# Kernel optimization log

Measured on AMD Instinct MI355X. Metric: run time of the kernel, lower is better.

## Reference

```python
import jax, jax.numpy as jnp
import numpy as np

FFT_NORM = "forward"


def _deq_cplx(qp, scale, mn):
    # qp stores (q_int8 + 127) in [0, 254]; dequant: qp*scale + min, last dim = (re, im)
    f = qp.astype(jnp.float32) * scale + mn
    return jax.lax.complex(f[..., 0], f[..., 1])


def setup_inputs() -> dict:
    key = jax.random.key(0)
    ks = jax.random.split(key, 16)
    B, Cin, Cout, H, W = 8, 32, 32, 256, 256
    NxW, NyW = 32, 17            # half-modes of the spectral weight
    r0, r1, r2, r3 = 16, 16, 16, 9  # Tucker ranks
    inp = {
        "x": jax.random.normal(ks[0], (B, Cin, H, W), dtype=jnp.float32),
        "core_scale": jax.random.uniform(ks[1], (), jnp.float32, 0.001, 0.02),
        "core_min": jax.random.normal(ks[2], (), jnp.float32) * 0.1,
        "factor_scales": jax.random.uniform(ks[3], (4,), jnp.float32, 0.001, 0.02),
        "factor_mins": jax.random.normal(ks[4], (4,), jnp.float32) * 0.1,
        "b_scale": jax.random.uniform(ks[5], (), jnp.float32, 0.001, 0.02),
        "b_min": jax.random.normal(ks[6], (), jnp.float32) * 0.1,
        "q_core": jax.random.randint(ks[7], (r0, r1, r2, r3, 2), 0, 255, jnp.int32),
        "q_f0": jax.random.randint(ks[8], (Cin, r0, 2), 0, 255, jnp.int32),
        "q_f1": jax.random.randint(ks[9], (Cout, r1, 2), 0, 255, jnp.int32),
        "q_f2": jax.random.randint(ks[10], (NxW, r2, 2), 0, 255, jnp.int32),
        "q_f3": jax.random.randint(ks[11], (NyW, r3, 2), 0, 255, jnp.int32),
        "q_bias": jax.random.randint(ks[12], (Cout,), 0, 255, jnp.int32),
    }
    return inp


def reference(x, core_scale, core_min, factor_scales, factor_mins, b_scale, b_min,
              q_core, q_f0, q_f1, q_f2, q_f3, q_bias):
    # 1) rFFT over the last two (spatial) dims
    x_fft = jnp.fft.rfftn(x, axes=(-2, -1), norm=FFT_NORM)  # [B, Cin, Nx, Ny_r] c64

    # 2) dequantize Tucker core + factors, reconstruct complex weight via multi_mode_dot
    core = _deq_cplx(q_core, core_scale, core_min)                       # [r0,r1,r2,r3]
    F0 = _deq_cplx(q_f0, factor_scales[0], factor_mins[0])               # [Cin, r0]
    F1 = _deq_cplx(q_f1, factor_scales[1], factor_mins[1])               # [Cout, r1]
    F2 = _deq_cplx(q_f2, factor_scales[2], factor_mins[2])               # [NxW, r2]
    F3 = _deq_cplx(q_f3, factor_scales[3], factor_mins[3])               # [NyW, r3]
    W = jnp.einsum('ijkl,ai,bj,ck,dl->abcd', core, F0, F1, F2, F3)       # [Cin,Cout,NxW,NyW]

    B, Cin, Nx, Ny_r = x_fft.shape
    CinW, Cout, NxW, NyW = W.shape
    assert Cin == CinW

    # 3) centered-slice channel mixing (faithful to the original double loop)
    cx, nx_neg, nx_pos = Nx // 2, NxW // 2, NxW // 2 + NxW % 2
    cy, ny_neg, ny_pos = Ny_r // 2, NyW // 2, NyW // 2 + NyW % 2
    sx = slice(cx - nx_neg, cx + nx_pos)
    sy = slice(cy - ny_neg, cy + ny_pos)
    Wx = slice(0, nx_pos + nx_neg)
    Wy = slice(0, ny_pos + ny_neg)

    mixed = jnp.einsum('bixy,ioxy->boxy', x_fft[:, :, sx, sy], W[:, :, Wx, Wy])
    out_fft = jnp.zeros((B, Cout, Nx, Ny_r), dtype=x_fft.dtype).at[:, :, sx, sy].set(mixed)

    # 4) inverse rFFT back to the original spatial size
    x_out = jnp.fft.irfftn(out_fft, s=x.shape[2:], axes=(-2, -1), norm=FFT_NORM)

    # 5) dequantized bias (real)
    bias = q_bias.astype(jnp.float32) * b_scale + b_min
    return x_out + bias[None, :, None, None]
```

## Files before the change

kernel.cpp:

```cpp
#include <hip/hip_runtime.h>


__device__ __forceinline__ float2 cfma(float2 a, float2 b, float2 c) {
    c.x = fmaf(a.x, b.x, fmaf(-a.y, b.y, c.x));
    c.y = fmaf(a.x, b.y, fmaf(a.y, b.x, c.y));
    return c;
}
__device__ __forceinline__ float2 cmul(float2 a, float2 b) {
    return make_float2(a.x*b.x - a.y*b.y, a.x*b.y + a.y*b.x);
}

__global__ __launch_bounds__(256) void wprep_kernel(
    const int* __restrict__ q_core, const int* __restrict__ q_f3,
    const float* __restrict__ core_scale, const float* __restrict__ core_min,
    const float* __restrict__ f_scales, const float* __restrict__ f_mins,
    float2* __restrict__ CL)
{
    int d = blockIdx.x >> 4, k = blockIdx.x & 15;
    int ij = threadIdx.x;
    float cs = *core_scale, cm = *core_min;
    float s3 = f_scales[3], m3 = f_mins[3];
    const int* qc = q_core + ((ij*16 + k)*9)*2;
    float2 acc = make_float2(0.f, 0.f);
#pragma unroll
    for (int l = 0; l < 9; ++l) {
        int2 q = *(const int2*)(qc + l*2);
        float2 ce = make_float2(q.x*cs + cm, q.y*cs + cm);
        float2 f3 = make_float2(q_f3[(d*9+l)*2]*s3 + m3, q_f3[(d*9+l)*2+1]*s3 + m3);
        acc = cfma(ce, f3, acc);
    }
    CL[(d*16 + k)*256 + ij] = acc;
}

__global__ __launch_bounds__(256) void weights_kernel(
    const float2* __restrict__ CL, const int* __restrict__ q_f0,
    const int* __restrict__ q_f1, const int* __restrict__ q_f2,
    const float* __restrict__ f_scales, const float* __restrict__ f_mins,
    float2* __restrict__ W4)
{
    __shared__ float2 F0s[512], F1s[512];
    __shared__ float2 C2p[16*17];
    __shared__ float2 A2p[16*33];
    int t = threadIdx.x, m = blockIdx.x;
    int c = m / 17, d = m % 17;
    float s0 = f_scales[0], m0 = f_mins[0];
    float s1 = f_scales[1], m1 = f_mins[1];
    float s2 = f_scales[2], m2 = f_mins[2];

    for (int e = t; e < 512; e += 256) {
        F0s[e] = make_float2(q_f0[2*e]*s0 + m0, q_f0[2*e+1]*s0 + m0);
        F1s[e] = make_float2(q_f1[2*e]*s1 + m1, q_f1[2*e+1]*s1 + m1);
    }
    {
        float2 acc = make_float2(0.f, 0.f);
#pragma unroll
        for (int k = 0; k < 16; ++k) {
            float2 clv = CL[(d*16 + k)*256 + t];
            float2 f2 = make_float2(q_f2[(c*16+k)*2]*s2 + m2,
                                    q_f2[(c*16+k)*2+1]*s2 + m2);
            acc = cfma(clv, f2, acc);
        }
        __syncthreads();
        C2p[(t >> 4)*17 + (t & 15)] = acc;
    }
    __syncthreads();
#pragma unroll
    for (int r = 0; r < 2; ++r) {
        int e = t + r*256; int i = e & 15, b = e >> 4;
        float2 acc = make_float2(0.f, 0.f);
#pragma unroll
        for (int j = 0; j < 16; ++j)
            acc = cfma(C2p[i*17 + j], F1s[b*16 + j], acc);
        A2p[i*33 + b] = acc;
    }
    __syncthreads();
    {
        int b = t & 31, a0 = t >> 5;
#pragma unroll
        for (int q = 0; q < 4; ++q) {
            int a = a0 + 8*q;
            float2 acc = make_float2(0.f, 0.f);
#pragma unroll
            for (int i = 0; i < 16; ++i)
                acc = cfma(F0s[a*16 + i], A2p[i*33 + b], acc);
            W4[m*1024 + a*32 + b] = acc;
        }
    }
}

__global__ __launch_bounds__(256) void fwd_w_kernel(const float* __restrict__ x,
                                                    float2* __restrict__ A1)
{
    __shared__ float ys0[64*65], ys2[64*65], yd02[64*65], yd13[64*65];
    __shared__ float2 twl[17*64];
    int tid = threadIdx.x;
    int row0 = blockIdx.x * 64;

    for (int i = tid; i < 17*64; i += 256) {
        int ki = i >> 6, wp = i & 63;
        int n = ((56 + ki) * wp) & 255;
        float a = n * (1.f/128.f);
        twl[i] = make_float2(cospif(a), -sinpif(a));
    }
    const float2* xf2 = (const float2*)x;
    for (int i2 = tid; i2 < 2048; i2 += 256) {
        int r = i2 >> 5, w2 = i2 & 31;
        const float2* xb = xf2 + (size_t)(row0 + r) * 128 + w2;
        float2 a0 = xb[0], a1 = xb[32], a2 = xb[64], a3 = xb[96];
        int ad = (2*w2)*65 + r;
        float s02 = a0.x + a2.x, s13 = a1.x + a3.x;
        ys0[ad] = s02 + s13;  ys2[ad] = s02 - s13;
        yd02[ad] = a0.x - a2.x;  yd13[ad] = a1.x - a3.x;
        s02 = a0.y + a2.y;  s13 = a1.y + a3.y;
        ys0[ad+65] = s02 + s13;  ys2[ad+65] = s02 - s13;
        yd02[ad+65] = a0.y - a2.y;  yd13[ad+65] = a1.y - a3.y;
    }
    __syncthreads();

    int lane = tid & 63, g = tid >> 6;
    int row = row0 + lane;
    if (g == 0) {
        float2 acc[5] = {};
        for (int wp = 0; wp < 64; ++wp) {
            float y = ys0[wp*65 + lane];
#pragma unroll
            for (int j = 0; j < 5; ++j) {
                float2 t = twl[(4*j)*64 + wp];
                acc[j].x = fmaf(y, t.x, acc[j].x);
                acc[j].y = fmaf(y, t.y, acc[j].y);
            }
        }
#pragma unroll
        for (int j = 0; j < 5; ++j) A1[(4*j)*65536 + row] = acc[j];
    } else if (g == 2) {
        float2 acc[4] = {};
        for (int wp = 0; wp < 64; ++wp) {
            float y = ys2[wp*65 + lane];
#pragma unroll
            for (int j = 0; j < 4; ++j) {
                float2 t = twl[(2+4*j)*64 + wp];
                acc[j].x = fmaf(y, t.x, acc[j].x);
                acc[j].y = fmaf(y, t.y, acc[j].y);
            }
        }
#pragma unroll
        for (int j = 0; j < 4; ++j) A1[(2+4*j)*65536 + row] = acc[j];
    } else if (g == 1) {
        float2 acc[4] = {};
        for (int wp = 0; wp < 64; ++wp) {
            float a = yd02[wp*65 + lane], b = yd13[wp*65 + lane];
#pragma unroll
            for (int j = 0; j < 4; ++j) {
                float2 t = twl[(1+4*j)*64 + wp];
                acc[j].x = fmaf(t.x, a, fmaf( t.y, b, acc[j].x));
                acc[j].y = fmaf(t.y, a, fmaf(-t.x, b, acc[j].y));
            }
        }
#pragma unroll
        for (int j = 0; j < 4; ++j) A1[(1+4*j)*65536 + row] = acc[j];
    } else {
        float2 acc[4] = {};
        for (int wp = 0; wp < 64; ++wp) {
            float a = yd02[wp*65 + lane], b = yd13[wp*65 + lane];
#pragma unroll
            for (int j = 0; j < 4; ++j) {
                float2 t = twl[(3+4*j)*64 + wp];
                acc[j].x = fmaf(t.x, a, fmaf(-t.y, b, acc[j].x));
                acc[j].y = fmaf(t.y, a, fmaf( t.x, b, acc[j].y));
            }
        }
#pragma unroll
        for (int j = 0; j < 4; ++j) A1[(3+4*j)*65536 + row] = acc[j];
    }
}

__global__ __launch_bounds__(256) void fwd_h_kernel(const float2* __restrict__ A1,
                                                    float2* __restrict__ X)
{
    __shared__ float2 tbl[256];
    __shared__ float as_re[8*264];
    __shared__ float as_im[8*264];
    int tid = threadIdx.x;
    int ky = blockIdx.x >> 5, bi0 = (blockIdx.x & 31) * 8;
    tbl[tid] = make_float2(cospif(tid * (1.f/128.f)), -sinpif(tid * (1.f/128.f)));
    for (int idx = tid; idx < 2048; idx += 256) {
        int b = idx >> 8, h = idx & 255;
        float2 v = A1[ky*65536 + (bi0 + b)*256 + h];
        int ad = (h >> 5)*264 + (h & 31)*8 + b;
        as_re[ad] = v.x; as_im[ad] = v.y;
    }
    __syncthreads();
    int lane = tid & 63, g = tid >> 6;
    int bl = lane & 7, q = lane >> 3;
    int kx0 = g * 8;
    float2 acc[8];
#pragma unroll
    for (int j = 0; j < 8; ++j) acc[j] = make_float2(0.f, 0.f);
    int base = q*264 + bl;
    for (int hh = 0; hh < 32; ++hh) {
        float ar = as_re[base + hh*8];
        float ai = as_im[base + hh*8];
#pragma unroll
        for (int j = 0; j < 8; ++j) {
            int kk = kx0 + j + 112;
            float2 t = tbl[(kk * hh) & 255];
            acc[j].x = fmaf(ar, t.x, fmaf(-ai, t.y, acc[j].x));
            acc[j].y = fmaf(ar, t.y, fmaf( ai, t.x, acc[j].y));
        }
    }
    float2 fstep = tbl[q * 32];
    float2 f = make_float2(1.f, 0.f);
#pragma unroll
    for (int j = 0; j < 8; ++j) {
        float2 v = cmul(acc[j], f);
        v.x += __shfl_xor(v.x, 8);  v.y += __shfl_xor(v.y, 8);
        v.x += __shfl_xor(v.x, 16); v.y += __shfl_xor(v.y, 16);
        v.x += __shfl_xor(v.x, 32); v.y += __shfl_xor(v.y, 32);
        acc[j] = v;
        f = cmul(f, fstep);
    }
    if (q == 0) {
        const float inv = 1.f / 65536.f;
#pragma unroll
        for (int j = 0; j < 8; ++j)
            X[((kx0 + j)*17 + ky)*256 + bi0 + bl] =
                make_float2(acc[j].x * inv, acc[j].y * inv);
    }
}

__global__ __launch_bounds__(256) void mix_kernel(const float2* __restrict__ X,
                                                  const float2* __restrict__ W4,
                                                  float2* __restrict__ Mx)
{
    __shared__ float2 Xs[256];
    __shared__ float2 Ws[1024];
    int tid = threadIdx.x, mode = blockIdx.x;
    Xs[tid] = X[mode*256 + tid];
    for (int idx = tid; idx < 1024; idx += 256) Ws[idx] = W4[mode*1024 + idx];
    __syncthreads();
    int b = tid >> 5, o = tid & 31;
    float2 acc = make_float2(0.f, 0.f);
#pragma unroll
    for (int i = 0; i < 32; ++i)
        acc = cfma(Xs[b*32 + i], Ws[i*32 + o], acc);
    Mx[mode*256 + tid] = acc;
}

template<int KY0, int NK>
__device__ __forceinline__ void invh_part(int h, int hh, const float2* ms, float2* Ts)
{
    float2 acc[NK];
#pragma unroll
    for (int j = 0; j < NK; ++j) acc[j] = make_float2(0.f, 0.f);
    int n0 = (112 * h) & 255;
    float tr = cospif(n0 * (1.f/128.f)), ti = sinpif(n0 * (1.f/128.f));
    float sr = cospif(h  * (1.f/128.f)), si = sinpif(h  * (1.f/128.f));
    for (int kx = 0; kx < 32; ++kx) {
#pragma unroll
        for (int j = 0; j < NK; ++j) {
            float2 mv = ms[kx*17 + KY0 + j];
            acc[j].x = fmaf(mv.x, tr, fmaf(-mv.y, ti, acc[j].x));
            acc[j].y = fmaf(mv.x, ti, fmaf( mv.y, tr, acc[j].y));
        }
        float ntr = fmaf(tr, sr, -ti*si);
        ti = fmaf(tr, si, ti*sr);
        tr = ntr;
    }
#pragma unroll
    for (int j = 0; j < NK; ++j) Ts[hh*18 + KY0 + j] = acc[j];
}

__global__ __launch_bounds__(256) void inv_kernel(const float2* __restrict__ Mx,
                                                  const int* __restrict__ q_bias,
                                                  const float* __restrict__ b_scale,
                                                  const float* __restrict__ b_min,
                                                  float* __restrict__ out)
{
    __shared__ float2 ms[544];
    __shared__ __align__(16) float2 Ts[32*18];
    int tid = threadIdx.x;
    int bo = blockIdx.x & 255, hc = blockIdx.x >> 8;
    for (int idx = tid; idx < 544; idx += 256) ms[idx] = Mx[idx*256 + bo];
    __syncthreads();
    {
        int hh = tid & 31, g = tid >> 5;
        int h = hc*32 + hh;
        if (g < 7) {
            switch (g) {
                case 0: invh_part<0, 2>(h, hh, ms, Ts); break;
                case 1: invh_part<2, 2>(h, hh, ms, Ts); break;
                case 2: invh_part<4, 2>(h, hh, ms, Ts); break;
                case 3: invh_part<6, 2>(h, hh, ms, Ts); break;
                case 4: invh_part<8, 2>(h, hh, ms, Ts); break;
                case 5: invh_part<10,2>(h, hh, ms, Ts); break;
                default:invh_part<12,2>(h, hh, ms, Ts); break;
            }
        } else {
            invh_part<14,3>(h, hh, ms, Ts);
        }
    }
    __syncthreads();
    {
        int w0 = tid & 63, hs = tid >> 6;
        float C[17], S[17];
        {
            int n0 = (56 * w0) & 255;
            float tr = cospif(n0 * (1.f/128.f)), ti = sinpif(n0 * (1.f/128.f));
            float sr = cospif(w0 * (1.f/128.f)), si = sinpif(w0 * (1.f/128.f));
#pragma unroll
            for (int ky = 0; ky < 17; ++ky) {
                C[ky] = tr; S[ky] = ti;
                float ntr = fmaf(tr, sr, -ti*si);
                ti = fmaf(tr, si, ti*sr);
                tr = ntr;
            }
        }
        float bias = q_bias[bo & 31] * (*b_scale) + (*b_min);
        float* obase = out + (size_t)bo*65536 + (size_t)hc*32*256;

#pragma unroll
        for (int r = 0; r < 8; ++r) {
            int hh = hs*8 + r;
            const float4* tp = (const float4*)&Ts[hh*18];
            float R0 = 0.f, R1 = 0.f, R2 = 0.f, R3 = 0.f, I1 = 0.f, I3 = 0.f;
#pragma unroll
            for (int kp = 0; kp < 9; ++kp) {
                float vx0, vy0, vx1 = 0.f, vy1 = 0.f;
                if (kp < 8) {
                    float4 v4 = tp[kp];
                    vx0 = v4.x; vy0 = v4.y; vx1 = v4.z; vy1 = v4.w;
                } else {
                    float2 v2 = Ts[hh*18 + 16];
                    vx0 = v2.x; vy0 = v2.y;
                }
#pragma unroll
                for (int half = 0; half < 2; ++half) {
                    if (kp == 8 && half == 1) break;
                    const int ky = 2*kp + half;
                    float vx = half ? vx1 : vx0;
                    float vy = half ? vy1 : vy0;
                    float ur = fmaf(vx, C[ky], -vy*S[ky]);
                    if ((ky & 1) == 0) {
                        if ((ky & 3) == 0) R0 += ur; else R2 += ur;
                    } else {
                        float ui = fmaf(vx, S[ky], vy*C[ky]);
                        if ((ky & 3) == 1) { R1 += ur; I1 += ui; }
                        else               { R3 += ur; I3 += ui; }
                    }
                }
            }
            float e02 = R0 + R2, d02 = R0 - R2;
            float e13 = R1 + R3, di  = I3 - I1;
            float q0 = e02 + e13, q2 = e02 - e13;
            float q1 = d02 + di,  q3 = d02 - di;
            obase[hh*256 + w0]       = fmaf(2.f, q0, bias);
            obase[hh*256 + w0 + 64]  = fmaf(2.f, q1, bias);
            obase[hh*256 + w0 + 128] = fmaf(2.f, q2, bias);
            obase[hh*256 + w0 + 192] = fmaf(2.f, q3, bias);
        }
    }
}

extern "C" void kernel_launch(void* const* d_in, const int* in_sizes, int n_in,
                              void* d_out, int out_size, void* d_ws, size_t ws_size,
                              hipStream_t stream) {
    const float* x          = (const float*)d_in[0];
    const float* core_scale = (const float*)d_in[1];
    const float* core_min   = (const float*)d_in[2];
    const float* f_scales   = (const float*)d_in[3];
    const float* f_mins     = (const float*)d_in[4];
    const float* b_scale    = (const float*)d_in[5];
    const float* b_min      = (const float*)d_in[6];
    const int* q_core = (const int*)d_in[7];
    const int* q_f0   = (const int*)d_in[8];
    const int* q_f1   = (const int*)d_in[9];
    const int* q_f2   = (const int*)d_in[10];
    const int* q_f3   = (const int*)d_in[11];
    const int* q_bias = (const int*)d_in[12];
    float* out = (float*)d_out;

    float2* ws = (float2*)d_ws;
    float2* A1 = ws;
    float2* W4 = ws + 1114112;
    float2* X  = W4 + 557056;
    float2* Mx = X + 139264;
    float2* CL = Mx + 139264;
    (void)ws_size; (void)n_in; (void)in_sizes; (void)out_size;

    wprep_kernel<<<272, 256, 0, stream>>>(q_core, q_f3, core_scale, core_min,
                                          f_scales, f_mins, CL);
    weights_kernel<<<544, 256, 0, stream>>>(CL, q_f0, q_f1, q_f2,
                                            f_scales, f_mins, W4);
    fwd_w_kernel<<<1024, 256, 0, stream>>>(x, A1);
    fwd_h_kernel<<<544, 256, 0, stream>>>(A1, X);
    mix_kernel<<<544, 256, 0, stream>>>(X, W4, Mx);
    inv_kernel<<<2048, 256, 0, stream>>>(Mx, q_bias, b_scale, b_min, out);
}
```

Measured before the change: 196.0 us.

## Fuse weight prep into weights kernel, vectorize twiddle loads, regroup inverse-H warps

Removes the separate wprep kernel and its CL buffer by precomputing the F2⊗F3 outer product per block in shared memory and contracting the raw quantized core directly. This drops a launch and a global round trip but makes each block redo the full core contraction (144 terms per thread). Also unrolls the forward W-pass by two and reads twiddles as float4, and restructures the inverse H-pass so each 64-lane wave handles two ky streams with shared twiddle recurrence instead of 32-thread templated groups.

```diff
diff --git a/kernel.cpp b/kernel.cpp
--- a/kernel.cpp
+++ b/kernel.cpp
@@ -10,35 +10,16 @@
     return make_float2(a.x*b.x - a.y*b.y, a.x*b.y + a.y*b.x);
 }
 
-__global__ __launch_bounds__(256) void wprep_kernel(
-    const int* __restrict__ q_core, const int* __restrict__ q_f3,
+__global__ __launch_bounds__(256) void weights_kernel(
+    const int* __restrict__ q_core, const int* __restrict__ q_f0,
+    const int* __restrict__ q_f1, const int* __restrict__ q_f2,
+    const int* __restrict__ q_f3,
     const float* __restrict__ core_scale, const float* __restrict__ core_min,
-    const float* __restrict__ f_scales, const float* __restrict__ f_mins,
-    float2* __restrict__ CL)
-{
-    int d = blockIdx.x >> 4, k = blockIdx.x & 15;
-    int ij = threadIdx.x;
-    float cs = *core_scale, cm = *core_min;
-    float s3 = f_scales[3], m3 = f_mins[3];
-    const int* qc = q_core + ((ij*16 + k)*9)*2;
-    float2 acc = make_float2(0.f, 0.f);
-#pragma unroll
-    for (int l = 0; l < 9; ++l) {
-        int2 q = *(const int2*)(qc + l*2);
-        float2 ce = make_float2(q.x*cs + cm, q.y*cs + cm);
-        float2 f3 = make_float2(q_f3[(d*9+l)*2]*s3 + m3, q_f3[(d*9+l)*2+1]*s3 + m3);
-        acc = cfma(ce, f3, acc);
-    }
-    CL[(d*16 + k)*256 + ij] = acc;
-}
-
-__global__ __launch_bounds__(256) void weights_kernel(
-    const float2* __restrict__ CL, const int* __restrict__ q_f0,
-    const int* __restrict__ q_f1, const int* __restrict__ q_f2,
     const float* __restrict__ f_scales, const float* __restrict__ f_mins,
     float2* __restrict__ W4)
 {
     __shared__ float2 F0s[512], F1s[512];
+    __shared__ float2 Gs[144];
     __shared__ float2 C2p[16*17];
     __shared__ float2 A2p[16*33];
     int t = threadIdx.x, m = blockIdx.x;
@@ -46,21 +27,33 @@
     float s0 = f_scales[0], m0 = f_mins[0];
     float s1 = f_scales[1], m1 = f_mins[1];
     float s2 = f_scales[2], m2 = f_mins[2];
+    float s3 = f_scales[3], m3 = f_mins[3];
+    float cs = *core_scale, cm = *core_min;
 
     for (int e = t; e < 512; e += 256) {
         F0s[e] = make_float2(q_f0[2*e]*s0 + m0, q_f0[2*e+1]*s0 + m0);
         F1s[e] = make_float2(q_f1[2*e]*s1 + m1, q_f1[2*e+1]*s1 + m1);
     }
+    if (t < 144) {
+        int k = t / 9, l = t - 9*k;
+        float2 f2 = make_float2(q_f2[(c*16+k)*2]*s2 + m2,
+                                q_f2[(c*16+k)*2+1]*s2 + m2);
+        float2 f3 = make_float2(q_f3[(d*9+l)*2]*s3 + m3,
+                                q_f3[(d*9+l)*2+1]*s3 + m3);
+        Gs[t] = cmul(f2, f3);
+    }
+    __syncthreads();
     {
+        const int4* qc = (const int4*)(q_core + t*288);
         float2 acc = make_float2(0.f, 0.f);
-#pragma unroll
-        for (int k = 0; k < 16; ++k) {
-            float2 clv = CL[(d*16 + k)*256 + t];
-            float2 f2 = make_float2(q_f2[(c*16+k)*2]*s2 + m2,
-                                    q_f2[(c*16+k)*2+1]*s2 + m2);
-            acc = cfma(clv, f2, acc);
-        }
-        __syncthreads();
+#pragma unroll 8
+        for (int p = 0; p < 72; ++p) {
+            int4 q = qc[p];
+            float2 ce0 = make_float2(q.x*cs + cm, q.y*cs + cm);
+            float2 ce1 = make_float2(q.z*cs + cm, q.w*cs + cm);
+            acc = cfma(ce0, Gs[2*p], acc);
+            acc = cfma(ce1, Gs[2*p+1], acc);
+        }
         C2p[(t >> 4)*17 + (t & 15)] = acc;
     }
     __syncthreads();
@@ -92,7 +85,7 @@
                                                     float2* __restrict__ A1)
 {
     __shared__ float ys0[64*65], ys2[64*65], yd02[64*65], yd13[64*65];
-    __shared__ float2 twl[17*64];
+    __shared__ __align__(16) float2 twl[17*64];
     int tid = threadIdx.x;
     int row0 = blockIdx.x * 64;
 
@@ -121,52 +114,64 @@
     int row = row0 + lane;
     if (g == 0) {
         float2 acc[5] = {};
-        for (int wp = 0; wp < 64; ++wp) {
-            float y = ys0[wp*65 + lane];
+#pragma unroll 2
+        for (int wp = 0; wp < 64; wp += 2) {
+            float ya = ys0[wp*65 + lane];
+            float yb = ys0[(wp+1)*65 + lane];
 #pragma unroll
             for (int j = 0; j < 5; ++j) {
-                float2 t = twl[(4*j)*64 + wp];
-                acc[j].x = fmaf(y, t.x, acc[j].x);
-                acc[j].y = fmaf(y, t.y, acc[j].y);
+                float4 tt = *(const float4*)&twl[(4*j)*64 + wp];
+                acc[j].x = fmaf(ya, tt.x, fmaf(yb, tt.z, acc[j].x));
+                acc[j].y = fmaf(ya, tt.y, fmaf(yb, tt.w, acc[j].y));
             }
         }
 #pragma unroll
         for (int j = 0; j < 5; ++j) A1[(4*j)*65536 + row] = acc[j];
     } else if (g == 2) {
         float2 acc[4] = {};
-        for (int wp = 0; wp < 64; ++wp) {
-            float y = ys2[wp*65 + lane];
+#pragma unroll 2
+        for (int wp = 0; wp < 64; wp += 2) {
+            float ya = ys2[wp*65 + lane];
+            float yb = ys2[(wp+1)*65 + lane];
 #pragma unroll
             for (int j = 0; j < 4; ++j) {
-                float2 t = twl[(2+4*j)*64 + wp];
-                acc[j].x = fmaf(y, t.x, acc[j].x);
-                acc[j].y = fmaf(y, t.y, acc[j].y);
+                float4 tt = *(const float4*)&twl[(2+4*j)*64 + wp];
+                acc[j].x = fmaf(ya, tt.x, fmaf(yb, tt.z, acc[j].x));
+                acc[j].y = fmaf(ya, tt.y, fmaf(yb, tt.w, acc[j].y));
             }
         }
 #pragma unroll
         for (int j = 0; j < 4; ++j) A1[(2+4*j)*65536 + row] = acc[j];
     } else if (g == 1) {
         float2 acc[4] = {};
-        for (int wp = 0; wp < 64; ++wp) {
-            float a = yd02[wp*65 + lane], b = yd13[wp*65 + lane];
+#pragma unroll 2
+        for (int wp = 0; wp < 64; wp += 2) {
+            float aa = yd02[wp*65 + lane],     ba = yd13[wp*65 + lane];
+            float ab = yd02[(wp+1)*65 + lane], bb = yd13[(wp+1)*65 + lane];
 #pragma unroll
             for (int j = 0; j < 4; ++j) {
-                float2 t = twl[(1+4*j)*64 + wp];
-                acc[j].x = fmaf(t.x, a, fmaf( t.y, b, acc[j].x));
-                acc[j].y = fmaf(t.y, a, fmaf(-t.x, b, acc[j].y));
+                float4 tt = *(const float4*)&twl[(1+4*j)*64 + wp];
+                acc[j].x = fmaf(tt.x, aa, fmaf( tt.y, ba,
+                           fmaf(tt.z, ab, fmaf( tt.w, bb, acc[j].x))));
+                acc[j].y = fmaf(tt.y, aa, fmaf(-tt.x, ba,
+                           fmaf(tt.w, ab, fmaf(-tt.z, bb, acc[j].y))));
             }
         }
 #pragma unroll
         for (int j = 0; j < 4; ++j) A1[(1+4*j)*65536 + row] = acc[j];
     } else {
         float2 acc[4] = {};
-        for (int wp = 0; wp < 64; ++wp) {
-            float a = yd02[wp*65 + lane], b = yd13[wp*65 + lane];
+#pragma unroll 2
+        for (int wp = 0; wp < 64; wp += 2) {
+            float aa = yd02[wp*65 + lane],     ba = yd13[wp*65 + lane];
+            float ab = yd02[(wp+1)*65 + lane], bb = yd13[(wp+1)*65 + lane];
 #pragma unroll
             for (int j = 0; j < 4; ++j) {
-                float2 t = twl[(3+4*j)*64 + wp];
-                acc[j].x = fmaf(t.x, a, fmaf(-t.y, b, acc[j].x));
-                acc[j].y = fmaf(t.y, a, fmaf( t.x, b, acc[j].y));
+                float4 tt = *(const float4*)&twl[(3+4*j)*64 + wp];
+                acc[j].x = fmaf(tt.x, aa, fmaf(-tt.y, ba,
+                           fmaf(tt.z, ab, fmaf(-tt.w, bb, acc[j].x))));
+                acc[j].y = fmaf(tt.y, aa, fmaf( tt.x, ba,
+                           fmaf(tt.w, ab, fmaf( tt.z, bb, acc[j].y))));
             }
         }
 #pragma unroll
@@ -246,30 +251,6 @@
     Mx[mode*256 + tid] = acc;
 }
 
-template<int KY0, int NK>
-__device__ __forceinline__ void invh_part(int h, int hh, const float2* ms, float2* Ts)
-{
-    float2 acc[NK];
-#pragma unroll
-    for (int j = 0; j < NK; ++j) acc[j] = make_float2(0.f, 0.f);
-    int n0 = (112 * h) & 255;
-    float tr = cospif(n0 * (1.f/128.f)), ti = sinpif(n0 * (1.f/128.f));
-    float sr = cospif(h  * (1.f/128.f)), si = sinpif(h  * (1.f/128.f));
-    for (int kx = 0; kx < 32; ++kx) {
-#pragma unroll
-        for (int j = 0; j < NK; ++j) {
-            float2 mv = ms[kx*17 + KY0 + j];
-            acc[j].x = fmaf(mv.x, tr, fmaf(-mv.y, ti, acc[j].x));
-            acc[j].y = fmaf(mv.x, ti, fmaf( mv.y, tr, acc[j].y));
-        }
-        float ntr = fmaf(tr, sr, -ti*si);
-        ti = fmaf(tr, si, ti*sr);
-        tr = ntr;
-    }
-#pragma unroll
-    for (int j = 0; j < NK; ++j) Ts[hh*18 + KY0 + j] = acc[j];
-}
-
 __global__ __launch_bounds__(256) void inv_kernel(const float2* __restrict__ Mx,
                                                   const int* __restrict__ q_bias,
                                                   const float* __restrict__ b_scale,
@@ -283,20 +264,49 @@
     for (int idx = tid; idx < 544; idx += 256) ms[idx] = Mx[idx*256 + bo];
     __syncthreads();
     {
-        int hh = tid & 31, g = tid >> 5;
+        int lane = tid & 63, w = tid >> 6;
+        int hh = lane & 31, ks = lane >> 5;
         int h = hc*32 + hh;
-        if (g < 7) {
-            switch (g) {
-                case 0: invh_part<0, 2>(h, hh, ms, Ts); break;
-                case 1: invh_part<2, 2>(h, hh, ms, Ts); break;
-                case 2: invh_part<4, 2>(h, hh, ms, Ts); break;
-                case 3: invh_part<6, 2>(h, hh, ms, Ts); break;
-                case 4: invh_part<8, 2>(h, hh, ms, Ts); break;
-                case 5: invh_part<10,2>(h, hh, ms, Ts); break;
-                default:invh_part<12,2>(h, hh, ms, Ts); break;
-            }
+        int n0 = (112 * h) & 255;
+        float tr = cospif(n0 * (1.f/128.f)), ti = sinpif(n0 * (1.f/128.f));
+        float sr = cospif(h  * (1.f/128.f)), si = sinpif(h  * (1.f/128.f));
+        if (w < 3) {
+            int ky0 = 4*w + ks;
+            float2 a0 = make_float2(0.f,0.f), a1 = make_float2(0.f,0.f);
+            for (int kx = 0; kx < 32; ++kx) {
+                const float2* mr = ms + kx*17;
+                float2 v0 = mr[ky0], v1 = mr[ky0+2];
+                a0.x = fmaf(v0.x, tr, fmaf(-v0.y, ti, a0.x));
+                a0.y = fmaf(v0.x, ti, fmaf( v0.y, tr, a0.y));
+                a1.x = fmaf(v1.x, tr, fmaf(-v1.y, ti, a1.x));
+                a1.y = fmaf(v1.x, ti, fmaf( v1.y, tr, a1.y));
+                float ntr = fmaf(tr, sr, -ti*si);
+                ti = fmaf(tr, si, ti*sr);
+                tr = ntr;
+            }
+            Ts[hh*18 + ky0]     = a0;
+            Ts[hh*18 + ky0 + 2] = a1;
         } else {
-            invh_part<14,3>(h, hh, ms, Ts);
+            int ky0 = 12 + ks;
+            int ky2 = ky0 + 4, ky2c = ky2 > 16 ? 16 : ky2;
+            float2 a0 = make_float2(0.f,0.f), a1 = make_float2(0.f,0.f),
+                   a2 = make_float2(0.f,0.f);
+            for (int kx = 0; kx < 32; ++kx) {
+                const float2* mr = ms + kx*17;
+                float2 v0 = mr[ky0], v1 = mr[ky0+2], v2 = mr[ky2c];
+                a0.x = fmaf(v0.x, tr, fmaf(-v0.y, ti, a0.x));
+                a0.y = fmaf(v0.x, ti, fmaf( v0.y, tr, a0.y));
+                a1.x = fmaf(v1.x, tr, fmaf(-v1.y, ti, a1.x));
+                a1.y = fmaf(v1.x, ti, fmaf( v1.y, tr, a1.y));
+                a2.x = fmaf(v2.x, tr, fmaf(-v2.y, ti, a2.x));
+                a2.y = fmaf(v2.x, ti, fmaf( v2.y, tr, a2.y));
+                float ntr = fmaf(tr, sr, -ti*si);
+                ti = fmaf(tr, si, ti*sr);
+                tr = ntr;
+            }
+            Ts[hh*18 + ky0]     = a0;
+            Ts[hh*18 + ky0 + 2] = a1;
+            if (ky2 < 17) Ts[hh*18 + ky2] = a2;
         }
     }
     __syncthreads();
@@ -384,12 +394,10 @@
     float2* W4 = ws + 1114112;
     float2* X  = W4 + 557056;
     float2* Mx = X + 139264;
-    float2* CL = Mx + 139264;
     (void)ws_size; (void)n_in; (void)in_sizes; (void)out_size;
 
-    wprep_kernel<<<272, 256, 0, stream>>>(q_core, q_f3, core_scale, core_min,
-                                          f_scales, f_mins, CL);
-    weights_kernel<<<544, 256, 0, stream>>>(CL, q_f0, q_f1, q_f2,
+    weights_kernel<<<544, 256, 0, stream>>>(q_core, q_f0, q_f1, q_f2, q_f3,
+                                            core_scale, core_min,
                                             f_scales, f_mins, W4);
     fwd_w_kernel<<<1024, 256, 0, stream>>>(x, A1);
     fwd_h_kernel<<<544, 256, 0, stream>>>(A1, X);
```

New measurement: 206.2 us. +5.2%, slower.
